# Kernel tuning notes

Hardware: AMD Instinct MI355X
Metric: run time of the kernel (lower is better)

The kernel has to match this reference:

```python
import jax, jax.numpy as jnp
import numpy as np

TEXT_DIM = 1024
FEAT_DIM = 1024
NUM_HEADS = 16
HEAD_DIM = FEAT_DIM // NUM_HEADS
EPS = 1e-6


def rms_norm(x, w):
    # LlamaRMSNorm: compute in fp32, scale by learned weight
    xf = x.astype(jnp.float32)
    var = jnp.mean(xf * xf, axis=-1, keepdims=True)
    return (xf * jax.lax.rsqrt(var + EPS)).astype(x.dtype) * w


def setup_inputs() -> dict:
    key = jax.random.key(0)
    ks = jax.random.split(key, 8)
    def xavier(k, shape, gain=1.0):
        fan_in, fan_out = shape[1], shape[0]
        lim = gain * np.sqrt(6.0 / (fan_in + fan_out))
        return jax.random.uniform(k, shape, jnp.float32, -lim, lim)
    return {
        "text": jax.random.normal(ks[0], (8, 512, TEXT_DIM), jnp.float32),
        "features": jax.random.normal(ks[1], (8, 1024, FEAT_DIM), jnp.float32),
        "W_q": xavier(ks[2], (FEAT_DIM, TEXT_DIM)),
        "b_q": jnp.zeros((FEAT_DIM,), jnp.float32),
        "W_k": xavier(ks[3], (FEAT_DIM, FEAT_DIM)),
        "b_k": jnp.zeros((FEAT_DIM,), jnp.float32),
        "W_o": xavier(ks[4], (FEAT_DIM, FEAT_DIM), gain=0.1),
        "b_o": jnp.zeros((FEAT_DIM,), jnp.float32),
        "g_feat": jnp.ones((FEAT_DIM,), jnp.float32),
        "g_q": jnp.ones((FEAT_DIM,), jnp.float32),
        "g_k": jnp.ones((FEAT_DIM,), jnp.float32),
    }


def reference(text, features, W_q, b_q, W_k, b_k, W_o, b_o, g_feat, g_q, g_k):
    B, T, _ = text.shape
    _, N, _ = features.shape
    feats = rms_norm(features, g_feat)                      # [B,N,Df]
    Q = rms_norm(text @ W_q.T + b_q, g_q)                   # [B,T,Df]
    K = rms_norm(feats @ W_k.T + b_k, g_k)                  # [B,N,Df]
    Qh = Q.reshape(B, T, NUM_HEADS, HEAD_DIM)
    Kh = K.reshape(B, N, NUM_HEADS, HEAD_DIM)
    Vh = feats.reshape(B, N, NUM_HEADS, HEAD_DIM)
    scores = jnp.einsum("bthd,bnhd->bhtn", Qh, Kh) / np.sqrt(HEAD_DIM).astype(np.float32)
    attn = jax.nn.softmax(scores, axis=-1)                  # [B,H,T,N]
    out = jnp.einsum("bhtn,bnhd->bthd", attn, Vh).reshape(B, T, FEAT_DIM)
    return out @ W_o.T + b_o
```

## Files before the change

kernel.cpp:

```cpp
#include <hip/hip_runtime.h>
#include <hip/hip_bf16.h>


typedef unsigned short u16;
typedef __bf16 bf16x8 __attribute__((ext_vector_type(8)));
typedef float f32x4 __attribute__((ext_vector_type(4)));

extern "C" __device__ float __ocml_native_exp2_f32(float);

__device__ inline f32x4 mfma16(bf16x8 a, bf16x8 b, f32x4 c) {
    return __builtin_amdgcn_mfma_f32_16x16x32_bf16(a, b, c, 0, 0, 0);
}

__device__ inline u16 f2bf(float f) {
    union { float f; unsigned u; } v; v.f = f;
    unsigned r = v.u + 0x7fffu + ((v.u >> 16) & 1u);
    return (u16)(r >> 16);
}

__device__ inline float bf2f(u16 x) {
    union { unsigned u; float f; } v; v.u = ((unsigned)x) << 16; return v.f;
}

__device__ inline unsigned pk_bf16(float a, float b) {
    union { float f; unsigned u; } x, y; x.f = a; y.f = b;
    return __builtin_amdgcn_perm(y.u + 0x8000u, x.u + 0x8000u, 0x07060302u);
}

__device__ inline void load_lds16(const void* g, void* l) {
    __builtin_amdgcn_global_load_lds(
        (const __attribute__((address_space(1))) void*)g,
        (__attribute__((address_space(3))) void*)l, 16, 0, 0);
}

__global__ __launch_bounds__(256) void cast_rows_kernel(const float* __restrict__ text,
                                                        const float* __restrict__ Wq,
                                                        const float* __restrict__ Wk,
                                                        const float* __restrict__ Wo,
                                                        const float* __restrict__ features,
                                                        u16* __restrict__ otext, u16* __restrict__ oWq,
                                                        u16* __restrict__ oWk, u16* __restrict__ oWo,
                                                        float* __restrict__ ssbuf,
                                                        float* __restrict__ qkss) {
    int blk = blockIdx.x, tid = threadIdx.x;
    if (blk < 7168) {
        int i = blk * 256 + tid;
        const float* src; u16* dst; int off;
        if (i < 1048576)      { src = text; dst = otext; off = i; }
        else if (i < 1310720) { src = Wq;   dst = oWq;   off = i - 1048576; }
        else if (i < 1572864) { src = Wk;   dst = oWk;   off = i - 1310720; }
        else                  { src = Wo;   dst = oWo;   off = i - 1572864; }
        float4 v = ((const float4*)src)[off];
        uint2 p; p.x = pk_bf16(v.x, v.y); p.y = pk_bf16(v.z, v.w);
        ((uint2*)dst)[off] = p;
    } else {
        int i2 = (blk - 7168) * 256 + tid;
        if (i2 < 12288) qkss[i2] = 0.0f;
        int row = (blk - 7168) * 4 + (tid >> 6);
        int lane = tid & 63;
        const float4* rp = (const float4*)(features + (size_t)row * 1024) + lane * 4;
        float ss = 0.0f;
        #pragma unroll
        for (int i = 0; i < 4; ++i) {
            float4 v = rp[i];
            ss += v.x * v.x + v.y * v.y + v.z * v.z + v.w * v.w;
        }
        #pragma unroll
        for (int m = 1; m < 64; m <<= 1) ss += __shfl_xor(ss, m, 64);
        if (lane == 0) ssbuf[row] = ss;
    }
}

__global__ __launch_bounds__(256) void normT_kernel(const float* __restrict__ features,
                                                    const float* __restrict__ ssbuf,
                                                    const float* __restrict__ g,
                                                    u16* __restrict__ feats_bf,
                                                    u16* __restrict__ Vt) {
    __shared__ __align__(16) u16 tile[64][72];
    int tid = threadIdx.x, b = blockIdx.z;
    int n0 = blockIdx.x * 64, d0 = blockIdx.y * 64;
    int r = tid >> 2, cs = (tid & 3) * 16;
    int grow = b * 1024 + n0 + r;

    float rs = rsqrtf(ssbuf[grow] * (1.0f / 1024.0f) + 1e-6f);
    const float4* src = (const float4*)(features + (size_t)grow * 1024 + d0 + cs);
    const float4* gp  = (const float4*)(g + d0 + cs);
    union { u16 s[16]; uint4 v[2]; } ob;
    #pragma unroll
    for (int i = 0; i < 4; ++i) {
        float4 v = src[i], gv = gp[i];
        unsigned lo = pk_bf16(v.x * rs * gv.x, v.y * rs * gv.y);
        unsigned hi = pk_bf16(v.z * rs * gv.z, v.w * rs * gv.w);
        ((unsigned*)ob.s)[i * 2]     = lo;
        ((unsigned*)ob.s)[i * 2 + 1] = hi;
    }
    uint4* dst = (uint4*)(feats_bf + (size_t)grow * 1024 + d0 + cs);
    dst[0] = ob.v[0]; dst[1] = ob.v[1];
    #pragma unroll
    for (int i = 0; i < 16; ++i) tile[r][cs + i] = ob.s[i];
    __syncthreads();
    union { u16 s[8]; uint4 v; } t0, t1;
    #pragma unroll
    for (int i = 0; i < 8; ++i) { t0.s[i] = tile[cs + i][r]; t1.s[i] = tile[cs + 8 + i][r]; }
    u16* tdst = Vt + ((size_t)(b * 1024 + d0 + r)) * 1024 + n0 + cs;
    *(uint4*)tdst = t0.v;
    *(uint4*)(tdst + 8) = t1.v;
}

template <bool BF16OUT, bool NORM>
__device__ __forceinline__ void gemm64_bk64(const u16* __restrict__ A, const u16* __restrict__ B,
                                            const float* __restrict__ bias,
                                            const float* __restrict__ gvec,
                                            float* __restrict__ ssout,
                                            void* __restrict__ Cout,
                                            int m_blk, int n_blk, int K, int N,
                                            u16* As, u16* Bs) {
    int tid = threadIdx.x, wave = tid >> 6, lane = tid & 63;
    int quad = lane >> 4, l15 = lane & 15;
    int wm = wave & 1, wn = wave >> 1;
    int srl = lane >> 3, scl = lane & 7;
    const int swz = (scl ^ srl) * 8;

    f32x4 acc[4][2] = {};

    auto stage = [&](int buf, int k0) {
        u16* Ad = As + buf * (128 * 64);
        u16* Bd = Bs + buf * (64 * 64);
        #pragma unroll
        for (int is = 0; is < 4; ++is) {
            int row = is * 32 + wave * 8 + srl;
            load_lds16(A + (size_t)(m_blk + row) * K + k0 + swz,
                       Ad + (is * 32 + wave * 8) * 64);
        }
        #pragma unroll
        for (int is = 0; is < 2; ++is) {
            int row = is * 32 + wave * 8 + srl;
            load_lds16(B + (size_t)(n_blk + row) * K + k0 + swz,
                       Bd + (is * 32 + wave * 8) * 64);
        }
    };

    stage(0, 0);
    __syncthreads();
    int cur = 0;

    for (int k0 = 0; k0 < K; k0 += 64) {
        if (k0 + 64 < K) stage(cur ^ 1, k0 + 64);

        const u16* Ar = As + cur * (128 * 64);
        const u16* Br = Bs + cur * (64 * 64);
        #pragma unroll
        for (int kh = 0; kh < 2; ++kh) {
            bf16x8 af[4], bfr[2];
            int co = ((kh * 4 + quad) ^ (l15 & 7)) * 8;
            #pragma unroll
            for (int t = 0; t < 4; ++t)
                af[t] = *(const bf16x8*)&Ar[(wm * 64 + t * 16 + l15) * 64 + co];
            #pragma unroll
            for (int t = 0; t < 2; ++t)
                bfr[t] = *(const bf16x8*)&Br[(wn * 32 + t * 16 + l15) * 64 + co];
            #pragma unroll
            for (int mt = 0; mt < 4; ++mt)
                #pragma unroll
                for (int nt = 0; nt < 2; ++nt)
                    acc[mt][nt] = mfma16(af[mt], bfr[nt], acc[mt][nt]);
        }
        __syncthreads();
        cur ^= 1;
    }

    float bv[2], gv[2];
    #pragma unroll
    for (int nt = 0; nt < 2; ++nt) {
        int col = n_blk + wn * 32 + nt * 16 + l15;
        bv[nt] = bias[col];
        if (NORM) gv[nt] = gvec[col];
    }
    #pragma unroll
    for (int mt = 0; mt < 4; ++mt) {
        int row0 = m_blk + wm * 64 + mt * 16 + quad * 4;
        #pragma unroll
        for (int nt = 0; nt < 2; ++nt)
            #pragma unroll
            for (int r = 0; r < 4; ++r)
                acc[mt][nt][r] += bv[nt];
        if (NORM) {
            f32x4 ss4 = {0.0f, 0.0f, 0.0f, 0.0f};
            #pragma unroll
            for (int nt = 0; nt < 2; ++nt)
                #pragma unroll
                for (int r = 0; r < 4; ++r)
                    ss4[r] += acc[mt][nt][r] * acc[mt][nt][r];
            #pragma unroll
            for (int m = 1; m < 16; m <<= 1)
                #pragma unroll
                for (int r = 0; r < 4; ++r)
                    ss4[r] += __shfl_xor(ss4[r], m, 64);
            if (l15 == 0) {
                #pragma unroll
                for (int r = 0; r < 4; ++r)
                    atomicAdd(&ssout[row0 + r], ss4[r]);
            }
        }
        #pragma unroll
        for (int nt = 0; nt < 2; ++nt) {
            int col = n_blk + wn * 32 + nt * 16 + l15;
            #pragma unroll
            for (int r = 0; r < 4; ++r) {
                float val = NORM ? acc[mt][nt][r] * gv[nt] : acc[mt][nt][r];
                if (BF16OUT) ((u16*)Cout)[(size_t)(row0 + r) * N + col] = f2bf(val);
                else       ((float*)Cout)[(size_t)(row0 + r) * N + col] = val;
            }
        }
    }
}

__global__ __launch_bounds__(256) void gemm_qk_kernel(const u16* __restrict__ text_bf,
                                                      const u16* __restrict__ Wq,
                                                      const u16* __restrict__ feats_bf,
                                                      const u16* __restrict__ Wk,
                                                      const float* __restrict__ b_q,
                                                      const float* __restrict__ b_k,
                                                      const float* __restrict__ g_q,
                                                      const float* __restrict__ g_k,
                                                      float* __restrict__ qkss,
                                                      u16* __restrict__ QK) {
    __shared__ __align__(16) u16 As[2 * 128 * 64];
    __shared__ __align__(16) u16 Bs[2 * 64 * 64];
    int id = blockIdx.x;
    if (id < 512) {
        gemm64_bk64<true, true>(text_bf, Wq, b_q, g_q, qkss, QK,
                                (id & 31) * 128, (id >> 5) * 64, 1024, 1024, As, Bs);
    } else {
        id -= 512;
        gemm64_bk64<true, true>(feats_bf, Wk, b_k, g_k, qkss + 4096, QK + 4096 * 1024,
                                (id & 63) * 128, (id >> 6) * 64, 1024, 1024, As, Bs);
    }
}

__global__ __launch_bounds__(256) void gemm_o_kernel(const u16* __restrict__ A,
                                                     const u16* __restrict__ B,
                                                     const float* __restrict__ bias,
                                                     float* __restrict__ C) {
    __shared__ __align__(16) u16 As[2 * 128 * 64];
    __shared__ __align__(16) u16 Bs[2 * 64 * 64];
    int id = blockIdx.x;
    gemm64_bk64<false, false>(A, B, bias, nullptr, nullptr, C,
                              (id & 31) * 128, (id >> 5) * 64, 1024, 1024, As, Bs);
}

__global__ __launch_bounds__(256, 4) void attn_kernel(const u16* __restrict__ Q,
                                                      const u16* __restrict__ K,
                                                      const u16* __restrict__ Vt,
                                                      const float* __restrict__ qkss,
                                                      u16* __restrict__ Out) {
    const float QSCALE = 0.18033688011112042f;
    int bh = blockIdx.x, qt = blockIdx.y;
    int b = bh >> 4, h = bh & 15;
    int tid = threadIdx.x, wave = tid >> 6, lane = tid & 63;
    int quad = lane >> 4, l15 = lane & 15;
    int wq = wave & 1, wn = wave >> 1;

    __shared__ __align__(16) u16 Ks[2][64 * 64];
    __shared__ __align__(16) u16 Vs[2][64 * 64];
    __shared__ __align__(16) u16 Plds[4][2 * 16 * 32];
    u16* Pw = &Plds[wave][0];
    const int pfs = (l15 >> 1) & 3;

    bf16x8 qf[2][2];
    float rsq[2];
    #pragma unroll
    for (int mt = 0; mt < 2; ++mt) {
        int qrow = b * 512 + qt * 64 + wq * 32 + mt * 16 + l15;
        const size_t qoff = (size_t)qrow * 1024 + h * 64 + quad * 8;
        qf[mt][0] = *(const bf16x8*)(Q + qoff);
        qf[mt][1] = *(const bf16x8*)(Q + qoff + 32);
        rsq[mt] = rsqrtf(qkss[qrow] * (1.0f / 1024.0f) + 1e-6f) * QSCALE;
    }
    const float* ssk = qkss + 4096 + b * 1024;

    int srl = lane >> 3, scl = lane & 7;
    const u16* Kbase = K + ((size_t)(b * 1024)) * 1024 + h * 64;
    const u16* Vbase = Vt + ((size_t)(b * 1024 + h * 64)) * 1024;

    __bf16 onev = (__bf16)1.0f;
    bf16x8 ones = {onev, onev, onev, onev, onev, onev, onev, onev};

    f32x4 o[2][4] = {};
    f32x4 lac[2] = {{0.0f, 0.0f, 0.0f, 0.0f}, {0.0f, 0.0f, 0.0f, 0.0f}};

    auto stage = [&](int buf, int n0) {
        #pragma unroll
        for (int j = 0; j < 2; ++j) {
            int row = wave * 16 + j * 8 + srl;
            load_lds16(Kbase + (size_t)(n0 + row) * 1024 + (scl ^ srl) * 8,
                       &Ks[buf][(wave * 16 + j * 8) * 64]);
            load_lds16(Vbase + (size_t)row * 1024 + n0 + (scl ^ srl) * 8,
                       &Vs[buf][(wave * 16 + j * 8) * 64]);
        }
    };

    stage(0, 0);
    __syncthreads();
    int cur = 0;

    for (int n0 = 0; n0 < 1024; n0 += 64) {
        if (n0 < 960) stage(cur ^ 1, n0 + 64);

        f32x4 s[2][2];
        __builtin_amdgcn_s_setprio(1);
        #pragma unroll
        for (int nt = 0; nt < 2; ++nt) {
            int R = wn * 32 + nt * 16 + l15;
            int c1 = (quad ^ (l15 & 7)) * 8;
            bf16x8 kf0 = *(const bf16x8*)&Ks[cur][R * 64 + c1];
            bf16x8 kf1 = *(const bf16x8*)&Ks[cur][R * 64 + (c1 ^ 32)];
            #pragma unroll
            for (int mt = 0; mt < 2; ++mt) {
                f32x4 z = {0.0f, 0.0f, 0.0f, 0.0f};
                s[mt][nt] = mfma16(kf0, qf[mt][0], z);
                s[mt][nt] = mfma16(kf1, qf[mt][1], s[mt][nt]);
            }
        }
        __builtin_amdgcn_s_setprio(0);

        #pragma unroll
        for (int nt = 0; nt < 2; ++nt) {
            int nb = n0 + wn * 32 + nt * 16 + quad * 4;
            f32x4 kss = *(const f32x4*)&ssk[nb];
            f32x4 rsn;
            #pragma unroll
            for (int r = 0; r < 4; ++r)
                rsn[r] = rsqrtf(kss[r] * (1.0f / 1024.0f) + 1e-6f);
            #pragma unroll
            for (int mt = 0; mt < 2; ++mt) {
                float e[4];
                #pragma unroll
                for (int r = 0; r < 4; ++r)
                    e[r] = __ocml_native_exp2_f32(fmaf(s[mt][nt][r], rsn[r] * rsq[mt], -16.0f));
                uint2 pk;
                pk.x = pk_bf16(e[0], e[1]);
                pk.y = pk_bf16(e[2], e[3]);
                *(uint2*)&Pw[mt * 512 + l15 * 32 + (((nt * 4 + quad) ^ (pfs << 1)) << 2)] = pk;
            }
        }

        bf16x8 pf[2], vf[4];
        #pragma unroll
        for (int mt = 0; mt < 2; ++mt)
            pf[mt] = *(const bf16x8*)&Pw[mt * 512 + l15 * 32 + ((quad ^ pfs) << 3)];
        #pragma unroll
        for (int dt = 0; dt < 4; ++dt) {
            int ch = ((wn * 4 + quad) ^ (l15 & 7)) * 8;
            vf[dt] = *(const bf16x8*)&Vs[cur][(dt * 16 + l15) * 64 + ch];
        }
        __builtin_amdgcn_s_setprio(1);
        #pragma unroll
        for (int mt = 0; mt < 2; ++mt) {
            lac[mt] = mfma16(ones, pf[mt], lac[mt]);
            #pragma unroll
            for (int dt = 0; dt < 4; ++dt)
                o[mt][dt] = mfma16(vf[dt], pf[mt], o[mt][dt]);
        }
        __builtin_amdgcn_s_setprio(0);

        __syncthreads();
        cur ^= 1;
    }

    float* Ored = (float*)&Ks[0][0];
    float* Lred = (float*)&Vs[0][0];
    if (wn == 1) {
        #pragma unroll
        for (int mt = 0; mt < 2; ++mt) {
            #pragma unroll
            for (int dt = 0; dt < 4; ++dt) {
                int c = mt * 4 + dt;
                *(f32x4*)&Ored[wq * 2048 + lane * 32 + ((c ^ (lane & 7)) << 2)] = o[mt][dt];
            }
            Lred[wq * 128 + lane * 2 + mt] = lac[mt][0];
        }
    }
    __syncthreads();
    if (wn == 0) {
        #pragma unroll
        for (int mt = 0; mt < 2; ++mt) {
            float il = 1.0f / (lac[mt][0] + Lred[wq * 128 + lane * 2 + mt]);
            size_t obase =
                ((size_t)(b * 512 + qt * 64 + wq * 32 + mt * 16 + l15)) * 1024 + h * 64 + quad * 4;
            #pragma unroll
            for (int dt = 0; dt < 4; ++dt) {
                int c = mt * 4 + dt;
                f32x4 oo = o[mt][dt] + *(const f32x4*)&Ored[wq * 2048 + lane * 32 + ((c ^ (lane & 7)) << 2)];
                uint2 pk;
                pk.x = pk_bf16(oo[0] * il, oo[1] * il);
                pk.y = pk_bf16(oo[2] * il, oo[3] * il);
                *(uint2*)(Out + obase + dt * 16) = pk;
            }
        }
    }
}

extern "C" void kernel_launch(void* const* d_in, const int* in_sizes, int n_in,
                              void* d_out, int out_size, void* d_ws, size_t ws_size,
                              hipStream_t stream) {
    const float* text     = (const float*)d_in[0];
    const float* features = (const float*)d_in[1];
    const float* W_q      = (const float*)d_in[2];
    const float* b_q      = (const float*)d_in[3];
    const float* W_k      = (const float*)d_in[4];
    const float* b_k      = (const float*)d_in[5];
    const float* W_o      = (const float*)d_in[6];
    const float* b_o      = (const float*)d_in[7];
    const float* g_feat   = (const float*)d_in[8];
    const float* g_q      = (const float*)d_in[9];
    const float* g_k      = (const float*)d_in[10];

    char* ws = (char*)d_ws;
    u16*   text_bf  = (u16*)(ws + 0);
    u16*   Wq_bf    = (u16*)(ws + 8388608);
    u16*   Wk_bf    = (u16*)(ws + 10485760);
    u16*   Wo_bf    = (u16*)(ws + 12582912);
    u16*   feats_bf = (u16*)(ws + 14680064);
    u16*   Vt       = (u16*)(ws + 31457280);
    u16*   QKbuf    = (u16*)(ws + 48234496);
    u16*   attn_bf  = (u16*)(ws + 73400320);
    float* ssbuf    = (float*)(ws + 81788928);
    float* qkss     = (float*)(ws + 81821696);

    cast_rows_kernel<<<9216, 256, 0, stream>>>(text, W_q, W_k, W_o, features,
                                               text_bf, Wq_bf, Wk_bf, Wo_bf, ssbuf, qkss);
    normT_kernel<<<dim3(16, 16, 8), 256, 0, stream>>>(features, ssbuf, g_feat, feats_bf, Vt);
    gemm_qk_kernel<<<1536, 256, 0, stream>>>(text_bf, Wq_bf, feats_bf, Wk_bf,
                                             b_q, b_k, g_q, g_k, qkss, QKbuf);
    attn_kernel<<<dim3(128, 8), 256, 0, stream>>>(QKbuf, QKbuf + 4096 * 1024, Vt, qkss, attn_bf);
    gemm_o_kernel<<<512, 256, 0, stream>>>(attn_bf, Wo_bf, b_o, (float*)d_out);
}
```

Baseline: 219.3 us.

## Triple-buffer GEMM LDS pipeline with vmcnt waits and XCD-aware block remap

Replaces the double-buffered GEMM main loop with a three-slot LDS ring. Each step waits with a partial vmcnt and a single barrier instead of a full syncthreads after compute, so global loads for step t+1 overlap with compute on step t. It also raises wave priority around the MFMA section and remaps block IDs so consecutive tiles land on the same XCD for L2 reuse. The cost is 50% more LDS per block, which may lower occupancy, and the single barrier is a possible hazard when a slot is overwritten.

```diff
diff --git a/kernel.cpp b/kernel.cpp
--- a/kernel.cpp
+++ b/kernel.cpp
@@ -123,32 +123,23 @@
 
     f32x4 acc[4][2] = {};
 
-    auto stage = [&](int buf, int k0) {
-        u16* Ad = As + buf * (128 * 64);
-        u16* Bd = Bs + buf * (64 * 64);
-        #pragma unroll
-        for (int is = 0; is < 4; ++is) {
-            int row = is * 32 + wave * 8 + srl;
-            load_lds16(A + (size_t)(m_blk + row) * K + k0 + swz,
+    auto stage = [&](int slot, int k0) {
+        u16* Ad = As + slot * (128 * 64);
+        u16* Bd = Bs + slot * (64 * 64);
+        #pragma unroll
+        for (int is = 0; is < 4; ++is)
+            load_lds16(A + (size_t)(m_blk + is * 32 + wave * 8 + srl) * K + k0 + swz,
                        Ad + (is * 32 + wave * 8) * 64);
-        }
-        #pragma unroll
-        for (int is = 0; is < 2; ++is) {
-            int row = is * 32 + wave * 8 + srl;
-            load_lds16(B + (size_t)(n_blk + row) * K + k0 + swz,
+        #pragma unroll
+        for (int is = 0; is < 2; ++is)
+            load_lds16(B + (size_t)(n_blk + is * 32 + wave * 8 + srl) * K + k0 + swz,
                        Bd + (is * 32 + wave * 8) * 64);
-        }
     };
 
-    stage(0, 0);
-    __syncthreads();
-    int cur = 0;
-
-    for (int k0 = 0; k0 < K; k0 += 64) {
-        if (k0 + 64 < K) stage(cur ^ 1, k0 + 64);
-
-        const u16* Ar = As + cur * (128 * 64);
-        const u16* Br = Bs + cur * (64 * 64);
+    auto compute = [&](int slot) {
+        const u16* Ar = As + slot * (128 * 64);
+        const u16* Br = Bs + slot * (64 * 64);
+        __builtin_amdgcn_s_setprio(1);
         #pragma unroll
         for (int kh = 0; kh < 2; ++kh) {
             bf16x8 af[4], bfr[2];
@@ -165,9 +156,23 @@
                 for (int nt = 0; nt < 2; ++nt)
                     acc[mt][nt] = mfma16(af[mt], bfr[nt], acc[mt][nt]);
         }
-        __syncthreads();
-        cur ^= 1;
-    }
+        __builtin_amdgcn_s_setprio(0);
+    };
+
+    const int nsteps = K >> 6;
+    stage(0, 0);
+    int cs = 0;
+    for (int t = 0; t < nsteps - 1; ++t) {
+        int ns = (cs == 2) ? 0 : cs + 1;
+        stage(ns, (t + 1) << 6);
+        asm volatile("s_waitcnt vmcnt(6)" ::: "memory");
+        __builtin_amdgcn_s_barrier();
+        compute(cs);
+        cs = ns;
+    }
+    asm volatile("s_waitcnt vmcnt(0)" ::: "memory");
+    __builtin_amdgcn_s_barrier();
+    compute(cs);
 
     float bv[2], gv[2];
     #pragma unroll
@@ -225,9 +230,9 @@
                                                       const float* __restrict__ g_k,
                                                       float* __restrict__ qkss,
                                                       u16* __restrict__ QK) {
-    __shared__ __align__(16) u16 As[2 * 128 * 64];
-    __shared__ __align__(16) u16 Bs[2 * 64 * 64];
-    int id = blockIdx.x;
+    __shared__ __align__(16) u16 As[3 * 128 * 64];
+    __shared__ __align__(16) u16 Bs[3 * 64 * 64];
+    int id = (blockIdx.x & 7) * 192 + (blockIdx.x >> 3);
     if (id < 512) {
         gemm64_bk64<true, true>(text_bf, Wq, b_q, g_q, qkss, QK,
                                 (id & 31) * 128, (id >> 5) * 64, 1024, 1024, As, Bs);
@@ -242,9 +247,9 @@
                                                      const u16* __restrict__ B,
                                                      const float* __restrict__ bias,
                                                      float* __restrict__ C) {
-    __shared__ __align__(16) u16 As[2 * 128 * 64];
-    __shared__ __align__(16) u16 Bs[2 * 64 * 64];
-    int id = blockIdx.x;
+    __shared__ __align__(16) u16 As[3 * 128 * 64];
+    __shared__ __align__(16) u16 Bs[3 * 64 * 64];
+    int id = (blockIdx.x & 7) * 64 + (blockIdx.x >> 3);
     gemm64_bk64<false, false>(A, B, bias, nullptr, nullptr, C,
                               (id & 31) * 128, (id >> 5) * 64, 1024, 1024, As, Bs);
 }
```

Result: slower. 247.6 us (+12.9%).

## Fuse feature RMSNorm into cast kernel and use hardware bf16 pack

Applied to the files above, without the earlier changes.

The feature RMSNorm moves into the row sum-of-squares pass, so the normalized bf16 features are written right away while the row is still in registers. The transpose kernel now reads bf16 features instead of re-reading fp32 features plus the norm scale, which roughly halves its input traffic and removes the ssbuf round trip. Separately, the attention kernel's bf16 packing switches to the v_cvt_pk_bf16_f32 instruction. That may round differently from the manual add-and-perm rounding used before.

```diff
diff --git a/kernel.cpp b/kernel.cpp
--- a/kernel.cpp
+++ b/kernel.cpp
@@ -18,13 +18,15 @@
     return (u16)(r >> 16);
 }
 
-__device__ inline float bf2f(u16 x) {
-    union { unsigned u; float f; } v; v.u = ((unsigned)x) << 16; return v.f;
-}
-
 __device__ inline unsigned pk_bf16(float a, float b) {
     union { float f; unsigned u; } x, y; x.f = a; y.f = b;
     return __builtin_amdgcn_perm(y.u + 0x8000u, x.u + 0x8000u, 0x07060302u);
+}
+
+__device__ inline unsigned cvt_pk(float a, float b) {
+    unsigned r;
+    asm("v_cvt_pk_bf16_f32 %0, %1, %2" : "=v"(r) : "v"(a), "v"(b));
+    return r;
 }
 
 __device__ inline void load_lds16(const void* g, void* l) {
@@ -38,9 +40,10 @@
                                                         const float* __restrict__ Wk,
                                                         const float* __restrict__ Wo,
                                                         const float* __restrict__ features,
+                                                        const float* __restrict__ g_feat,
                                                         u16* __restrict__ otext, u16* __restrict__ oWq,
                                                         u16* __restrict__ oWk, u16* __restrict__ oWo,
-                                                        float* __restrict__ ssbuf,
+                                                        u16* __restrict__ feats_bf,
                                                         float* __restrict__ qkss) {
     int blk = blockIdx.x, tid = threadIdx.x;
     if (blk < 7168) {
@@ -59,22 +62,31 @@
         int row = (blk - 7168) * 4 + (tid >> 6);
         int lane = tid & 63;
         const float4* rp = (const float4*)(features + (size_t)row * 1024) + lane * 4;
+        float4 v[4];
         float ss = 0.0f;
         #pragma unroll
         for (int i = 0; i < 4; ++i) {
-            float4 v = rp[i];
-            ss += v.x * v.x + v.y * v.y + v.z * v.z + v.w * v.w;
+            v[i] = rp[i];
+            ss += v[i].x * v[i].x + v[i].y * v[i].y + v[i].z * v[i].z + v[i].w * v[i].w;
         }
         #pragma unroll
         for (int m = 1; m < 64; m <<= 1) ss += __shfl_xor(ss, m, 64);
-        if (lane == 0) ssbuf[row] = ss;
-    }
-}
-
-__global__ __launch_bounds__(256) void normT_kernel(const float* __restrict__ features,
-                                                    const float* __restrict__ ssbuf,
-                                                    const float* __restrict__ g,
-                                                    u16* __restrict__ feats_bf,
+        float rs = rsqrtf(ss * (1.0f / 1024.0f) + 1e-6f);
+        const float4* gp = (const float4*)(g_feat) + lane * 4;
+        union { unsigned u[8]; uint4 q[2]; } ob;
+        #pragma unroll
+        for (int i = 0; i < 4; ++i) {
+            float4 gv = gp[i];
+            ob.u[i * 2]     = pk_bf16(v[i].x * rs * gv.x, v[i].y * rs * gv.y);
+            ob.u[i * 2 + 1] = pk_bf16(v[i].z * rs * gv.z, v[i].w * rs * gv.w);
+        }
+        uint4* dst = (uint4*)(feats_bf + (size_t)row * 1024 + lane * 16);
+        dst[0] = ob.q[0];
+        dst[1] = ob.q[1];
+    }
+}
+
+__global__ __launch_bounds__(256) void normT_kernel(const u16* __restrict__ feats_bf,
                                                     u16* __restrict__ Vt) {
     __shared__ __align__(16) u16 tile[64][72];
     int tid = threadIdx.x, b = blockIdx.z;
@@ -82,20 +94,10 @@
     int r = tid >> 2, cs = (tid & 3) * 16;
     int grow = b * 1024 + n0 + r;
 
-    float rs = rsqrtf(ssbuf[grow] * (1.0f / 1024.0f) + 1e-6f);
-    const float4* src = (const float4*)(features + (size_t)grow * 1024 + d0 + cs);
-    const float4* gp  = (const float4*)(g + d0 + cs);
+    const uint4* src = (const uint4*)(feats_bf + (size_t)grow * 1024 + d0 + cs);
     union { u16 s[16]; uint4 v[2]; } ob;
-    #pragma unroll
-    for (int i = 0; i < 4; ++i) {
-        float4 v = src[i], gv = gp[i];
-        unsigned lo = pk_bf16(v.x * rs * gv.x, v.y * rs * gv.y);
-        unsigned hi = pk_bf16(v.z * rs * gv.z, v.w * rs * gv.w);
-        ((unsigned*)ob.s)[i * 2]     = lo;
-        ((unsigned*)ob.s)[i * 2 + 1] = hi;
-    }
-    uint4* dst = (uint4*)(feats_bf + (size_t)grow * 1024 + d0 + cs);
-    dst[0] = ob.v[0]; dst[1] = ob.v[1];
+    ob.v[0] = src[0];
+    ob.v[1] = src[1];
     #pragma unroll
     for (int i = 0; i < 16; ++i) tile[r][cs + i] = ob.s[i];
     __syncthreads();
@@ -339,8 +341,8 @@
                 for (int r = 0; r < 4; ++r)
                     e[r] = __ocml_native_exp2_f32(fmaf(s[mt][nt][r], rsn[r] * rsq[mt], -16.0f));
                 uint2 pk;
-                pk.x = pk_bf16(e[0], e[1]);
-                pk.y = pk_bf16(e[2], e[3]);
+                pk.x = cvt_pk(e[0], e[1]);
+                pk.y = cvt_pk(e[2], e[3]);
                 *(uint2*)&Pw[mt * 512 + l15 * 32 + (((nt * 4 + quad) ^ (pfs << 1)) << 2)] = pk;
             }
         }
@@ -393,8 +395,8 @@
                 int c = mt * 4 + dt;
                 f32x4 oo = o[mt][dt] + *(const f32x4*)&Ored[wq * 2048 + lane * 32 + ((c ^ (lane & 7)) << 2)];
                 uint2 pk;
-                pk.x = pk_bf16(oo[0] * il, oo[1] * il);
-                pk.y = pk_bf16(oo[2] * il, oo[3] * il);
+                pk.x = cvt_pk(oo[0] * il, oo[1] * il);
+                pk.y = cvt_pk(oo[2] * il, oo[3] * il);
                 *(uint2*)(Out + obase + dt * 16) = pk;
             }
         }
@@ -425,12 +427,12 @@
     u16*   Vt       = (u16*)(ws + 31457280);
     u16*   QKbuf    = (u16*)(ws + 48234496);
     u16*   attn_bf  = (u16*)(ws + 73400320);
-    float* ssbuf    = (float*)(ws + 81788928);
     float* qkss     = (float*)(ws + 81821696);
 
-    cast_rows_kernel<<<9216, 256, 0, stream>>>(text, W_q, W_k, W_o, features,
-                                               text_bf, Wq_bf, Wk_bf, Wo_bf, ssbuf, qkss);
-    normT_kernel<<<dim3(16, 16, 8), 256, 0, stream>>>(features, ssbuf, g_feat, feats_bf, Vt);
+    cast_rows_kernel<<<9216, 256, 0, stream>>>(text, W_q, W_k, W_o, features, g_feat,
+                                               text_bf, Wq_bf, Wk_bf, Wo_bf,
+                                               feats_bf, qkss);
+    normT_kernel<<<dim3(16, 16, 8), 256, 0, stream>>>(feats_bf, Vt);
     gemm_qk_kernel<<<1536, 256, 0, stream>>>(text_bf, Wq_bf, feats_bf, Wk_bf,
                                              b_q, b_k, g_q, g_k, qkss, QKbuf);
     attn_kernel<<<dim3(128, 8), 256, 0, stream>>>(QKbuf, QKbuf + 4096 * 1024, Vt, qkss, attn_bf);
```

Measured after the change: 219.8 us. Within noise of the previous version (+0.3%).
